# Kernel optimization log

Hardware: AMD Instinct MI355X
Metric: run time of the kernel (lower is better)

The kernel has to match this reference:

```python
import jax, jax.numpy as jnp
import numpy as np
import math

B, T, D, H = 2, 4096, 1024, 16
DH = D // H
LOCAL = 3
MAX_GATE = 0.6


def dilated_positions(seq_len, local=LOCAL):
    A = local + int(math.ceil(math.log2(max(seq_len, 2)))) + 1
    pos = np.zeros((seq_len, A), np.int32)
    msk = np.zeros((seq_len, A), bool)
    for i in range(seq_len):
        ap = [i] + [i - j for j in range(1, local + 1) if i - j >= 0]
        k = 2
        while 2 ** k <= i:
            ap.append(i - 2 ** k)
            k += 1
        pos[i, :len(ap)] = ap
        msk[i, :len(ap)] = True
    return pos, msk


def pid_proj(x, Wp, Wi, Wd, Wg, bg):
    # x: (B,T,D); W*: (D,D); Wg: (D,3); bg: (3,)
    t = x.shape[1]
    denom = jnp.arange(1, t + 1, dtype=x.dtype)[None, :, None]
    integral = jnp.cumsum(x, axis=1) / denom
    derivative = jnp.concatenate([jnp.zeros_like(x[:, :1]), x[:, 1:] - x[:, :-1]], axis=1)
    g = jax.nn.softmax(x @ Wg + bg, axis=-1)
    g = jnp.minimum(g, MAX_GATE)
    g = g / g.sum(axis=-1, keepdims=True)
    return g[..., 0:1] * (x @ Wp) + g[..., 1:2] * (integral @ Wi) + g[..., 2:3] * (derivative @ Wd)


def setup_inputs() -> dict:
    key = jax.random.key(0)
    ks = jax.random.split(key, 16)
    s = 1.0 / math.sqrt(D)
    inp = {"x": jax.random.normal(ks[0], (B, T, D), jnp.float32)}
    i = 1
    for name in ("q", "k", "v"):
        inp[f"Wp_{name}"] = jax.random.normal(ks[i], (D, D), jnp.float32) * s; i += 1
        inp[f"Wi_{name}"] = jax.random.normal(ks[i], (D, D), jnp.float32) * s * 0.3; i += 1
        inp[f"Wd_{name}"] = jax.random.normal(ks[i], (D, D), jnp.float32) * s * 0.3; i += 1
        inp[f"Wg_{name}"] = jax.random.normal(ks[i], (D, 3), jnp.float32) * s; i += 1
        inp[f"bg_{name}"] = jnp.array([0.5, 0.0, 0.0], jnp.float32)
    inp["Wo"] = jax.random.normal(ks[13], (D, D), jnp.float32) * s
    pos, msk = dilated_positions(T)
    inp["positions"] = jnp.asarray(pos)
    inp["mask"] = jnp.asarray(msk)
    return inp


def reference(x, Wp_q, Wi_q, Wd_q, Wg_q, bg_q,
              Wp_k, Wi_k, Wd_k, Wg_k, bg_k,
              Wp_v, Wi_v, Wd_v, Wg_v, bg_v,
              Wo, positions, mask):
    b, t, d = x.shape
    scale = DH ** -0.5
    def heads(y):  # (B,T,D) -> (B,H,T,DH)
        return y.reshape(b, t, H, DH).transpose(0, 2, 1, 3)
    q = heads(pid_proj(x, Wp_q, Wi_q, Wd_q, Wg_q, bg_q))
    k = heads(pid_proj(x, Wp_k, Wi_k, Wd_k, Wg_k, bg_k))
    v = heads(pid_proj(x, Wp_v, Wi_v, Wd_v, Wg_v, bg_v))
    # gather per-query sparse K/V: (B,H,T,A,DH)
    k_sparse = k[:, :, positions]
    v_sparse = v[:, :, positions]
    scores = jnp.einsum('bhsd,bhsad->bhsa', q, k_sparse) * scale
    scores = jnp.where(mask[None, None], scores, -jnp.inf)
    attn = jax.nn.softmax(scores, axis=-1)
    out = jnp.einsum('bhsa,bhsad->bhsd', attn, v_sparse)
    out = out.transpose(0, 2, 1, 3).reshape(b, t, d)
    return out @ Wo
```

## Files before the change

kernel.cpp:

```cpp
#include <hip/hip_runtime.h>
#include <hip/hip_bf16.h>
#include <cstdint>

#define B_   2
#define T_   4096
#define D_   1024
#define H_   16
#define DH_  64
#define M_   (B_*T_)
#define K3_  (3*D_)
#define TC_  128
#define NCH_ (T_/TC_)

typedef __attribute__((ext_vector_type(4))) float  f32x4;
typedef __attribute__((ext_vector_type(8))) short  short8;

__device__ __forceinline__ float bf2f(ushort u) {
    union { uint32_t i; float f; } v; v.i = ((uint32_t)u) << 16; return v.f;
}
__device__ __forceinline__ ushort f2bf(float f) {
    union { float f; uint32_t i; } v; v.f = f;
    uint32_t r = v.i + 0x7FFF + ((v.i >> 16) & 1);
    return (ushort)(r >> 16);
}

template<bool F32>
__device__ __forceinline__ float ld_in(const void* p, size_t i) {
    if (F32) return ((const float*)p)[i];
    return bf2f(((const ushort*)p)[i]);
}

__device__ __forceinline__ void st_c(ushort* p, float v) { *p = f2bf(v); }
__device__ __forceinline__ void st_c(float*  p, float v) { *p = v; }

#define GLOAD_LDS16(g, l) \
    __builtin_amdgcn_global_load_lds((const __attribute__((address_space(1))) void*)(g), \
                                     (__attribute__((address_space(3))) void*)(l), 16, 0, 0)

__global__ void detect_kernel(const ushort* __restrict__ xu, int* __restrict__ flag) {
    __shared__ int cnt;
    if (threadIdx.x == 0) cnt = 0;
    __syncthreads();
    int c = 0;
    for (int i = threadIdx.x; i < 16384; i += 256) {
        ushort u = xu[i];
        if ((u & 0x7F80) == 0x7F80) c++;
    }
    if (c) atomicAdd(&cnt, c);
    __syncthreads();
    if (threadIdx.x == 0) flag[0] = (cnt > 0) ? 1 : 0;
}

template<bool F32>
__device__ __forceinline__ void gates_body(const void* x,
                                           const void* Wg_q, const void* bg_q,
                                           const void* Wg_k, const void* bg_k,
                                           const void* Wg_v, const void* bg_v,
                                           float* __restrict__ g9) {
    const int wave = threadIdx.x >> 6, lane = threadIdx.x & 63;
    const int row  = blockIdx.x * 4 + wave;
    const size_t xoff = (size_t)row * D_;
    float acc[9] = {0,0,0,0,0,0,0,0,0};
    for (int d = lane; d < D_; d += 64) {
        float xv = ld_in<F32>(x, xoff + d);
        #pragma unroll
        for (int c = 0; c < 3; c++) {
            acc[0+c] += xv * ld_in<F32>(Wg_q, d*3+c);
            acc[3+c] += xv * ld_in<F32>(Wg_k, d*3+c);
            acc[6+c] += xv * ld_in<F32>(Wg_v, d*3+c);
        }
    }
    #pragma unroll
    for (int i = 0; i < 9; i++) {
        #pragma unroll
        for (int o = 32; o >= 1; o >>= 1) acc[i] += __shfl_xor(acc[i], o, 64);
    }
    const void* bgs[3] = {bg_q, bg_k, bg_v};
    float g[9];
    #pragma unroll
    for (int p = 0; p < 3; p++) {
        float l0 = acc[p*3+0] + ld_in<F32>(bgs[p], 0);
        float l1 = acc[p*3+1] + ld_in<F32>(bgs[p], 1);
        float l2 = acc[p*3+2] + ld_in<F32>(bgs[p], 2);
        float mx = fmaxf(l0, fmaxf(l1, l2));
        float e0 = expf(l0-mx), e1 = expf(l1-mx), e2 = expf(l2-mx);
        float s  = e0+e1+e2;
        float g0 = fminf(e0/s, 0.6f), g1 = fminf(e1/s, 0.6f), g2 = fminf(e2/s, 0.6f);
        float s2 = g0+g1+g2;
        g0 /= s2; g1 /= s2; g2 /= s2;
        float g1c = fmaxf(g1, 1e-30f), g2c = fmaxf(g2, 1e-30f);
        g[p*3+0] = g0 / g1c;
        g[p*3+1] = g1c / g2c;
        g[p*3+2] = g2c;
    }
    if (lane == 0) {
        #pragma unroll
        for (int i = 0; i < 9; i++) g9[(size_t)row*9 + i] = g[i];
    }
}
__global__ void gates_kernel(const void* x,
                             const void* Wg_q, const void* bg_q,
                             const void* Wg_k, const void* bg_k,
                             const void* Wg_v, const void* bg_v,
                             const int* __restrict__ flag, float* __restrict__ g9) {
    if (flag[0]) gates_body<true >(x, Wg_q, bg_q, Wg_k, bg_k, Wg_v, bg_v, g9);
    else         gates_body<false>(x, Wg_q, bg_q, Wg_k, bg_k, Wg_v, bg_v, g9);
}

template<bool F32>
__device__ __forceinline__ void chunk_sum_body(const void* x, float* __restrict__ part) {
    const int d = blockIdx.x * 256 + threadIdx.x;
    const int tc = blockIdx.y, b = blockIdx.z;
    const size_t base = ((size_t)b*T_ + (size_t)tc*TC_) * D_ + d;
    float s = 0.f;
    for (int i = 0; i < TC_; i++) s += ld_in<F32>(x, base + (size_t)i * D_);
    part[((size_t)b*NCH_ + tc) * D_ + d] = s;
}
__global__ void chunk_sum_kernel(const void* x, const int* __restrict__ flag,
                                 float* __restrict__ part) {
    if (flag[0]) chunk_sum_body<true >(x, part);
    else         chunk_sum_body<false>(x, part);
}

__global__ void scan_part_kernel(float* __restrict__ part) {
    const int idx = blockIdx.x * 256 + threadIdx.x;
    const int b = idx >> 10, d = idx & (D_-1);
    float run = 0.f;
    for (int tc = 0; tc < NCH_; tc++) {
        size_t o = ((size_t)b*NCH_ + tc) * D_ + d;
        float v = part[o]; part[o] = run; run += v;
    }
}

template<bool F32>
__device__ __forceinline__ void build_xs_body(const void* x, const float* __restrict__ part,
                                              ushort* __restrict__ Xc) {
    const int d0 = (blockIdx.x * 256 + threadIdx.x) * 2;
    const int tc = blockIdx.y, b = blockIdx.z;
    const int t0 = tc * TC_;
    float carry0 = part[((size_t)b*NCH_ + tc) * D_ + d0];
    float carry1 = part[((size_t)b*NCH_ + tc) * D_ + d0 + 1];
    const size_t xbase = ((size_t)b*T_ + t0) * D_ + d0;
    float prev0 = (t0 > 0) ? ld_in<F32>(x, xbase - D_)     : 0.0f;
    float prev1 = (t0 > 0) ? ld_in<F32>(x, xbase - D_ + 1) : 0.0f;
    for (int i = 0; i < TC_; i++) {
        const int t = t0 + i;
        float xv0 = ld_in<F32>(x, xbase + (size_t)i * D_);
        float xv1 = ld_in<F32>(x, xbase + (size_t)i * D_ + 1);
        carry0 += xv0; carry1 += xv1;
        const float rinv = 1.0f / (float)(t + 1);
        float in0 = carry0 * rinv, in1 = carry1 * rinv;
        float de0 = (t == 0) ? 0.0f : (xv0 - prev0);
        float de1 = (t == 0) ? 0.0f : (xv1 - prev1);
        prev0 = xv0; prev1 = xv1;
        const size_t base = ((size_t)b*T_ + t) * K3_ + d0;
        *(ushort2*)(Xc + base       ) = make_ushort2(f2bf(xv0), f2bf(xv1));
        *(ushort2*)(Xc + base +   D_) = make_ushort2(f2bf(in0), f2bf(in1));
        *(ushort2*)(Xc + base + 2*D_) = make_ushort2(f2bf(de0), f2bf(de1));
    }
}
__global__ void build_xs_kernel(const void* x, const float* __restrict__ part,
                                const int* __restrict__ flag, ushort* __restrict__ Xc) {
    if (flag[0]) build_xs_body<true >(x, part, Xc);
    else         build_xs_body<false>(x, part, Xc);
}

struct WPtrs { const void* w[10]; };
template<bool F32>
__device__ __forceinline__ void transpose_w_body(WPtrs ptrs, ushort* __restrict__ Wt,
                                                 ushort* __restrict__ WoT) {
    const int z = blockIdx.z;
    const void* src = ptrs.w[z];
    __shared__ float tile[32][33];
    const int tx = threadIdx.x & 31, ty = threadIdx.x >> 5;
    const int d0 = blockIdx.x * 32, c0 = blockIdx.y * 32;
    #pragma unroll
    for (int i = 0; i < 4; i++) {
        int r = ty + i*8;
        tile[r][tx] = ld_in<F32>(src, (size_t)(d0 + r) * D_ + c0 + tx);
    }
    __syncthreads();
    if (z < 9) {
        const int p = z / 3, j = z % 3;
        #pragma unroll
        for (int i = 0; i < 4; i++) {
            int r = ty + i*8;
            Wt[(size_t)(p*D_ + c0 + r) * K3_ + j*D_ + d0 + tx] = f2bf(tile[tx][r]);
        }
    } else {
        #pragma unroll
        for (int i = 0; i < 4; i++) {
            int r = ty + i*8;
            WoT[(size_t)(c0 + r) * D_ + d0 + tx] = f2bf(tile[tx][r]);
        }
    }
}
__global__ void transpose_w_kernel(WPtrs ptrs, const int* __restrict__ flag,
                                   ushort* __restrict__ Wt, ushort* __restrict__ WoT) {
    if (flag[0]) transpose_w_body<true >(ptrs, Wt, WoT);
    else         transpose_w_body<false>(ptrs, Wt, WoT);
}

template<typename CT, int NTILES, bool GATED>
__global__ __launch_bounds__(512, 2) void gemm_bt8_kernel(
        const ushort* __restrict__ Abase,
        const ushort* __restrict__ Bt,
        CT* __restrict__ C,
        const float* __restrict__ g9,
        int K, int lda, int ldc) {
    __shared__ __align__(16) ushort LDS[3 * 24576];
    const int tid  = threadIdx.x;
    const int lane = tid & 63;
    const int wave = tid >> 6;
    const int wm   = wave >> 2;
    const int wn   = wave & 3;
    const int quad = lane >> 4, l16 = lane & 15, sw = l16 & 7;

    const int MT     = M_ / 128;
    const int cpx    = (MT * NTILES) / 8;
    const int wg     = (blockIdx.x % 8) * cpx + blockIdx.x / 8;
    const int mchunk = MT / 8;
    const int rem    = wg % (mchunk * NTILES);
    const int mt     = (wg / (mchunk * NTILES)) * mchunk + (rem % mchunk);
    const int nt     = rem / mchunk;
    const int m0 = mt * 128;
    const int n0 = nt * 256;
    const int p  = n0 >> 10;

    const ushort* asrc[2]; int aoff[2];
    #pragma unroll
    for (int g = 0; g < 2; g++) {
        const int I = g*512 + tid;
        const int row = I >> 3, c8 = (I & 7) ^ (row & 7);
        asrc[g] = Abase + (size_t)(m0 + row) * lda + c8*8;
        aoff[g] = I * 8;
    }
    const ushort* bsrc[4]; int boff[4];
    #pragma unroll
    for (int g = 0; g < 4; g++) {
        const int I = g*512 + tid;
        const int row = I >> 3, c8 = (I & 7) ^ (row & 7);
        bsrc[g] = Bt + (size_t)(n0 + row) * K + c8*8;
        boff[g] = I * 8;
    }
    int ard[4], brd[4];
    #pragma unroll
    for (int i = 0; i < 4; i++) {
        ard[i] = (wm*64 + i*16 + l16) * 64;
        brd[i] = (wn*64 + i*16 + l16) * 64;
    }

    const int NKT = K >> 6;
    f32x4 acc[4][4] = {};

    #pragma unroll
    for (int g = 0; g < 2; g++) GLOAD_LDS16(asrc[g], &LDS[aoff[g]]);
    #pragma unroll
    for (int g = 0; g < 4; g++) GLOAD_LDS16(bsrc[g], &LDS[8192 + boff[g]]);
    #pragma unroll
    for (int g = 0; g < 2; g++) GLOAD_LDS16(asrc[g] + 64, &LDS[24576 + aoff[g]]);
    #pragma unroll
    for (int g = 0; g < 4; g++) GLOAD_LDS16(bsrc[g] + 64, &LDS[24576 + 8192 + boff[g]]);
    asm volatile("s_waitcnt vmcnt(6)" ::: "memory");
    __builtin_amdgcn_s_barrier();

    for (int t = 0; t < NKT; ++t) {
        const int cur = t % 3;
        const int ab  = cur * 24576;
        const int bb  = ab + 8192;
        const bool do_stage = (t + 2 < NKT);
        const int sb  = ((t + 2) % 3) * 24576;
        const int skt = (t + 2) << 6;

        short8 af[4], bfr[4];

        #pragma unroll
        for (int i = 0; i < 4; i++)
            af[i]  = *(const short8*)&LDS[ab + ard[i] + (quad ^ sw) * 8];
        #pragma unroll
        for (int j = 0; j < 4; j++)
            bfr[j] = *(const short8*)&LDS[bb + brd[j] + (quad ^ sw) * 8];
        if (do_stage) {
            GLOAD_LDS16(asrc[0] + skt, &LDS[sb + aoff[0]]);
            GLOAD_LDS16(asrc[1] + skt, &LDS[sb + aoff[1]]);
            GLOAD_LDS16(bsrc[0] + skt, &LDS[sb + 8192 + boff[0]]);
        }
        __builtin_amdgcn_s_barrier();
        asm volatile("s_waitcnt lgkmcnt(0)" ::: "memory");
        __builtin_amdgcn_sched_barrier(0);
        __builtin_amdgcn_s_setprio(1);
        #pragma unroll
        for (int i = 0; i < 4; i++)
            #pragma unroll
            for (int j = 0; j < 4; j++)
                acc[i][j] = __builtin_amdgcn_mfma_f32_16x16x32_bf16(af[i], bfr[j], acc[i][j], 0, 0, 0);
        __builtin_amdgcn_s_setprio(0);
        __builtin_amdgcn_s_barrier();

        #pragma unroll
        for (int i = 0; i < 4; i++)
            af[i]  = *(const short8*)&LDS[ab + ard[i] + ((quad + 4) ^ sw) * 8];
        #pragma unroll
        for (int j = 0; j < 4; j++)
            bfr[j] = *(const short8*)&LDS[bb + brd[j] + ((quad + 4) ^ sw) * 8];
        if (do_stage) {
            GLOAD_LDS16(bsrc[1] + skt, &LDS[sb + 8192 + boff[1]]);
            GLOAD_LDS16(bsrc[2] + skt, &LDS[sb + 8192 + boff[2]]);
            GLOAD_LDS16(bsrc[3] + skt, &LDS[sb + 8192 + boff[3]]);
        }
        __builtin_amdgcn_s_barrier();
        asm volatile("s_waitcnt lgkmcnt(0)" ::: "memory");
        __builtin_amdgcn_sched_barrier(0);
        __builtin_amdgcn_s_setprio(1);
        #pragma unroll
        for (int i = 0; i < 4; i++)
            #pragma unroll
            for (int j = 0; j < 4; j++)
                acc[i][j] = __builtin_amdgcn_mfma_f32_16x16x32_bf16(af[i], bfr[j], acc[i][j], 0, 0, 0);
        __builtin_amdgcn_s_setprio(0);
        if (do_stage)          asm volatile("s_waitcnt vmcnt(6)" ::: "memory");
        else if (t + 1 < NKT)  asm volatile("s_waitcnt vmcnt(0)" ::: "memory");
        __builtin_amdgcn_s_barrier();

        if (GATED && ((t & 15) == 15)) {
            const int seg = t >> 4;
            #pragma unroll
            for (int i = 0; i < 4; i++) {
                float gv[4];
                #pragma unroll
                for (int rg = 0; rg < 4; rg++) {
                    const int rrow = m0 + wm*64 + i*16 + quad*4 + rg;
                    gv[rg] = g9[(size_t)rrow * 9 + p*3 + seg];
                }
                #pragma unroll
                for (int j = 0; j < 4; j++)
                    #pragma unroll
                    for (int rg = 0; rg < 4; rg++)
                        acc[i][j][rg] *= gv[rg];
            }
        }
    }

    #pragma unroll
    for (int i = 0; i < 4; i++) {
        #pragma unroll
        for (int j = 0; j < 4; j++) {
            const int rrow = m0 + wm*64 + i*16 + quad*4;
            const int col  = n0 + wn*64 + j*16 + l16;
            #pragma unroll
            for (int rg = 0; rg < 4; rg++)
                st_c(&C[(size_t)(rrow + rg) * ldc + col], acc[i][j][rg]);
        }
    }
}

__global__ __launch_bounds__(256) void attn_kernel(const ushort* __restrict__ QKV,
                                                   ushort* __restrict__ AO) {
    const int tid = threadIdx.x;
    const int bt  = blockIdx.x;
    const int t   = bt & (T_-1);
    const size_t qrow = (size_t)bt * K3_;
    const int e0 = tid * 4;

    const ushort4 q4 = *(const ushort4*)(QKV + qrow + e0);
    const float qf0 = bf2f(q4.x), qf1 = bf2f(q4.y), qf2 = bf2f(q4.z), qf3 = bf2f(q4.w);

    float sc[14];
    #pragma unroll
    for (int a = 0; a < 14; a++) {
        const int off = (a <= 3) ? a : (1 << (a - 2));
        float p = -1e30f;
        if (off <= t) {
            const ushort4 k4 = *(const ushort4*)(QKV + qrow - (size_t)off*K3_ + D_ + e0);
            float pp = qf0*bf2f(k4.x) + qf1*bf2f(k4.y) + qf2*bf2f(k4.z) + qf3*bf2f(k4.w);
            pp += __shfl_xor(pp, 1, 64);
            pp += __shfl_xor(pp, 2, 64);
            pp += __shfl_xor(pp, 4, 64);
            pp += __shfl_xor(pp, 8, 64);
            p = pp * 0.125f;
        }
        sc[a] = p;
    }
    float mx = -1e30f;
    #pragma unroll
    for (int a = 0; a < 14; a++) mx = fmaxf(mx, sc[a]);
    float ev[14], s = 0.0f;
    #pragma unroll
    for (int a = 0; a < 14; a++) { ev[a] = (sc[a] > -1e29f) ? expf(sc[a] - mx) : 0.0f; s += ev[a]; }
    const float rs = 1.0f / s;

    float a0 = 0.f, a1 = 0.f, a2 = 0.f, a3 = 0.f;
    #pragma unroll
    for (int a = 0; a < 14; a++) {
        const int off = (a <= 3) ? a : (1 << (a - 2));
        if (off <= t) {
            const ushort4 v4 = *(const ushort4*)(QKV + qrow - (size_t)off*K3_ + 2*D_ + e0);
            const float w = ev[a] * rs;
            a0 += w * bf2f(v4.x); a1 += w * bf2f(v4.y);
            a2 += w * bf2f(v4.z); a3 += w * bf2f(v4.w);
        }
    }
    ushort* dst = AO + (size_t)bt * D_ + e0;
    dst[0] = f2bf(a0); dst[1] = f2bf(a1); dst[2] = f2bf(a2); dst[3] = f2bf(a3);
}

extern "C" void kernel_launch(void* const* d_in, const int* in_sizes, int n_in,
                              void* d_out, int out_size, void* d_ws, size_t ws_size,
                              hipStream_t stream) {
    (void)in_sizes; (void)n_in; (void)out_size; (void)ws_size;
    const void* x    = d_in[0];
    const void* Wg_q = d_in[4];  const void* bg_q = d_in[5];
    const void* Wg_k = d_in[9];  const void* bg_k = d_in[10];
    const void* Wg_v = d_in[14]; const void* bg_v = d_in[15];

    char* ws = (char*)d_ws;
    int*    flag = (int*)ws;    ws += 16;
    float*  g9   = (float*)ws;  ws += (size_t)M_*9*4;
    float*  part = (float*)ws;  ws += (size_t)B_*NCH_*D_*4;
    ushort* Wt   = (ushort*)ws; ws += (size_t)K3_*K3_*2;
    ushort* WoT  = (ushort*)ws; ws += (size_t)D_*D_*2;
    ushort* Xc   = (ushort*)ws; ws += (size_t)M_*K3_*2;
    ushort* QKV  = (ushort*)ws; ws += (size_t)M_*K3_*2;
    ushort* AO   = (ushort*)ws; ws += (size_t)M_*D_*2;

    detect_kernel<<<1, 256, 0, stream>>>((const ushort*)x, flag);
    gates_kernel<<<M_/4, 256, 0, stream>>>(x, Wg_q, bg_q, Wg_k, bg_k, Wg_v, bg_v, flag, g9);
    chunk_sum_kernel<<<dim3(D_/256, NCH_, B_), 256, 0, stream>>>(x, flag, part);
    scan_part_kernel<<<(B_*D_)/256, 256, 0, stream>>>(part);
    WPtrs wp;
    wp.w[0] = d_in[1];  wp.w[1] = d_in[2];  wp.w[2] = d_in[3];
    wp.w[3] = d_in[6];  wp.w[4] = d_in[7];  wp.w[5] = d_in[8];
    wp.w[6] = d_in[11]; wp.w[7] = d_in[12]; wp.w[8] = d_in[13];
    wp.w[9] = d_in[16];
    transpose_w_kernel<<<dim3(32, 32, 10), 256, 0, stream>>>(wp, flag, Wt, WoT);
    build_xs_kernel<<<dim3(D_/512, NCH_, B_), 256, 0, stream>>>(x, part, flag, Xc);
    gemm_bt8_kernel<ushort, 12, true><<<768, 512, 0, stream>>>(Xc, Wt, QKV, g9, K3_, K3_, K3_);
    attn_kernel<<<B_*T_, 256, 0, stream>>>(QKV, AO);
    gemm_bt8_kernel<float, 4, false><<<256, 512, 0, stream>>>(AO, WoT, (float*)d_out, nullptr, D_, D_, D_);
}
```

Baseline: 481.3 us.

## Add dedicated 256x384-tile QKV GEMM kernel with split-phase staged pipeline

Replaces the generic 128-row QKV GEMM (768 blocks) with a specialised kernel that computes 256x384 output tiles per 512-thread block over 256 blocks. Each wave holds an 8x6 grid of 16x16 MFMA accumulators. The K loop runs a triple-buffered LDS pipeline whose global loads are split across two compute phases. The gate scaling is applied to the accumulators at each 1024-wide K segment boundary. The larger tile increases operand reuse and cuts global traffic, but it raises register pressure (192 accumulator floats per lane) and leaves only 256 blocks, which may underfill the GPU.

```diff
diff --git a/kernel.cpp b/kernel.cpp
--- a/kernel.cpp
+++ b/kernel.cpp
@@ -201,6 +201,136 @@
     else         transpose_w_body<false>(ptrs, Wt, WoT);
 }
 
+__global__ __launch_bounds__(512, 2) void gemm_qkv_kernel(
+        const ushort* __restrict__ Abase,
+        const ushort* __restrict__ Bt,
+        ushort* __restrict__ C,
+        const float* __restrict__ g9) {
+    constexpr int BUFE = 20480;
+    constexpr int NKT  = K3_ / 32;
+    __shared__ __align__(16) ushort LDS[3 * BUFE];
+    const int tid  = threadIdx.x;
+    const int lane = tid & 63;
+    const int wave = tid >> 6;
+    const int wm   = wave >> 2;
+    const int wn   = wave & 3;
+    const int quad = lane >> 4, l16 = lane & 15;
+
+    const int wg  = (blockIdx.x % 8) * 32 + blockIdx.x / 8;
+    const int rem = wg & 31;
+    const int mt  = (wg >> 5) * 4 + (rem & 3);
+    const int nt  = rem >> 2;
+    const int m0  = mt * 256;
+    const int n0  = nt * 384;
+
+    const ushort* gsrc[5]; int loff[5];
+    #pragma unroll
+    for (int g = 0; g < 5; g++) {
+        const int I = g*512 + tid;
+        if (I < 1024) {
+            gsrc[g] = Abase + (size_t)(m0 + (I >> 2)) * K3_ + (I & 3) * 8;
+            loff[g] = I * 8;
+        } else {
+            const int J = I - 1024;
+            gsrc[g] = Bt + (size_t)(n0 + (J >> 2)) * K3_ + (J & 3) * 8;
+            loff[g] = 8192 + J * 8;
+        }
+    }
+    int ard[8], brd[6];
+    #pragma unroll
+    for (int i = 0; i < 8; i++) ard[i] = (wm*128 + i*16 + l16) * 32 + quad*8;
+    #pragma unroll
+    for (int j = 0; j < 6; j++) brd[j] = 8192 + (wn*96 + j*16 + l16) * 32 + quad*8;
+
+    f32x4 acc[8][6] = {};
+
+    #pragma unroll
+    for (int g = 0; g < 5; g++) GLOAD_LDS16(gsrc[g], &LDS[loff[g]]);
+    #pragma unroll
+    for (int g = 0; g < 5; g++) GLOAD_LDS16(gsrc[g] + 32, &LDS[BUFE + loff[g]]);
+    asm volatile("s_waitcnt vmcnt(5)" ::: "memory");
+    __builtin_amdgcn_s_barrier();
+
+    for (int t = 0; t < NKT; ++t) {
+        const int bs = (t % 3) * BUFE;
+        const bool do_stage = (t + 2 < NKT);
+        const int sb = ((t + 2) % 3) * BUFE;
+        const int sk = (t + 2) * 32;
+
+        short8 af[4], bfr[6], af2[4];
+
+        #pragma unroll
+        for (int i = 0; i < 4; i++) af[i]  = *(const short8*)&LDS[bs + ard[i]];
+        #pragma unroll
+        for (int j = 0; j < 6; j++) bfr[j] = *(const short8*)&LDS[bs + brd[j]];
+        if (do_stage) {
+            GLOAD_LDS16(gsrc[0] + sk, &LDS[sb + loff[0]]);
+            GLOAD_LDS16(gsrc[1] + sk, &LDS[sb + loff[1]]);
+            GLOAD_LDS16(gsrc[2] + sk, &LDS[sb + loff[2]]);
+        }
+        __builtin_amdgcn_s_barrier();
+        asm volatile("s_waitcnt lgkmcnt(0)" ::: "memory");
+        __builtin_amdgcn_sched_barrier(0);
+        __builtin_amdgcn_s_setprio(1);
+        #pragma unroll
+        for (int i = 0; i < 4; i++)
+            #pragma unroll
+            for (int j = 0; j < 6; j++)
+                acc[i][j] = __builtin_amdgcn_mfma_f32_16x16x32_bf16(af[i], bfr[j], acc[i][j], 0, 0, 0);
+        __builtin_amdgcn_s_setprio(0);
+        __builtin_amdgcn_s_barrier();
+
+        #pragma unroll
+        for (int i = 0; i < 4; i++) af2[i] = *(const short8*)&LDS[bs + ard[i+4]];
+        if (do_stage) {
+            GLOAD_LDS16(gsrc[3] + sk, &LDS[sb + loff[3]]);
+            GLOAD_LDS16(gsrc[4] + sk, &LDS[sb + loff[4]]);
+        }
+        __builtin_amdgcn_s_barrier();
+        asm volatile("s_waitcnt lgkmcnt(0)" ::: "memory");
+        __builtin_amdgcn_sched_barrier(0);
+        __builtin_amdgcn_s_setprio(1);
+        #pragma unroll
+        for (int i = 0; i < 4; i++)
+            #pragma unroll
+            for (int j = 0; j < 6; j++)
+                acc[i+4][j] = __builtin_amdgcn_mfma_f32_16x16x32_bf16(af2[i], bfr[j], acc[i+4][j], 0, 0, 0);
+        __builtin_amdgcn_s_setprio(0);
+        if (do_stage)          asm volatile("s_waitcnt vmcnt(5)" ::: "memory");
+        else if (t + 1 < NKT)  asm volatile("s_waitcnt vmcnt(0)" ::: "memory");
+        __builtin_amdgcn_s_barrier();
+
+        if ((t & 31) == 31) {
+            const int seg = t >> 5;
+            #pragma unroll
+            for (int i = 0; i < 8; i++) {
+                #pragma unroll
+                for (int rg = 0; rg < 4; rg++) {
+                    const int rrow = m0 + wm*128 + i*16 + quad*4 + rg;
+                    const float* gr = &g9[(size_t)rrow * 9 + seg];
+                    #pragma unroll
+                    for (int j = 0; j < 6; j++) {
+                        const int pj = (n0 + wn*96 + j*16) >> 10;
+                        acc[i][j][rg] *= gr[pj*3];
+                    }
+                }
+            }
+        }
+    }
+
+    #pragma unroll
+    for (int i = 0; i < 8; i++) {
+        #pragma unroll
+        for (int j = 0; j < 6; j++) {
+            const int rrow = m0 + wm*128 + i*16 + quad*4;
+            const int col  = n0 + wn*96 + j*16 + l16;
+            #pragma unroll
+            for (int rg = 0; rg < 4; rg++)
+                C[(size_t)(rrow + rg) * K3_ + col] = f2bf(acc[i][j][rg]);
+        }
+    }
+}
+
 template<typename CT, int NTILES, bool GATED>
 __global__ __launch_bounds__(512, 2) void gemm_bt8_kernel(
         const ushort* __restrict__ Abase,
@@ -434,7 +564,7 @@
     wp.w[9] = d_in[16];
     transpose_w_kernel<<<dim3(32, 32, 10), 256, 0, stream>>>(wp, flag, Wt, WoT);
     build_xs_kernel<<<dim3(D_/512, NCH_, B_), 256, 0, stream>>>(x, part, flag, Xc);
-    gemm_bt8_kernel<ushort, 12, true><<<768, 512, 0, stream>>>(Xc, Wt, QKV, g9, K3_, K3_, K3_);
+    gemm_qkv_kernel<<<256, 512, 0, stream>>>(Xc, Wt, QKV, g9);
     attn_kernel<<<B_*T_, 256, 0, stream>>>(QKV, AO);
     gemm_bt8_kernel<float, 4, false><<<256, 512, 0, stream>>>(AO, WoT, (float*)d_out, nullptr, D_, D_, D_);
 }
```

Measured after the change: 566.3 us. +17.7%, slower.

## Add dedicated 256x256-tile QKV GEMM with 4-stage LDS pipeline and in-loop gating

Applied to the files above, without the earlier changes.

Replaces the generic gated GEMM for the fused QKV projection with a specialized kernel using 256x256 output tiles (384 workgroups instead of 768), a 4-deep LDS ring buffer with direct global-to-LDS loads, and swizzled LDS reads. Gate scaling is applied to the accumulators at each 1024-wide K segment boundary. The aim is higher arithmetic intensity per tile and better overlap of loads with MFMA work. In exchange it uses more registers and LDS per workgroup, and with fewer workgroups the 256 CUs are covered less evenly.

```diff
diff --git a/kernel.cpp b/kernel.cpp
--- a/kernel.cpp
+++ b/kernel.cpp
@@ -201,6 +201,131 @@
     else         transpose_w_body<false>(ptrs, Wt, WoT);
 }
 
+__global__ __launch_bounds__(512, 2) void gemm_qkv_kernel(
+        const ushort* __restrict__ Abase,
+        const ushort* __restrict__ Bt,
+        ushort* __restrict__ C,
+        const float* __restrict__ g9) {
+    constexpr int SUBE = 16384;
+    constexpr int NS   = K3_ / 32;
+    constexpr int RSTR = 128 * K3_;
+    __shared__ __align__(16) ushort LDS[4 * SUBE];
+    const int tid  = threadIdx.x;
+    const int lane = tid & 63;
+    const int wave = tid >> 6;
+    const int wm   = wave >> 2;
+    const int wn   = wave & 3;
+    const int quad = lane >> 4, l16 = lane & 15;
+    const int gq   = quad ^ ((l16 >> 1) & 3);
+
+    const int wg = (blockIdx.x % 8) * 48 + blockIdx.x / 8;
+    const int mt = wg & 31;
+    const int nt = wg >> 5;
+    const int m0 = mt * 256;
+    const int n0 = nt * 256;
+    const int p  = n0 >> 10;
+
+    const int arow = tid >> 2;
+    const int acg  = (tid & 3) ^ ((arow >> 1) & 3);
+    const ushort* pA = Abase + (size_t)(m0 + arow) * K3_ + acg * 8;
+    const ushort* pB = Bt    + (size_t)(n0 + arow) * K3_ + acg * 8;
+    const int l8 = tid * 8;
+
+    int ard[8], brd[4];
+    #pragma unroll
+    for (int i = 0; i < 8; i++) ard[i] = (wm*128 + i*16 + l16) * 32 + gq*8;
+    #pragma unroll
+    for (int j = 0; j < 4; j++) brd[j] = 8192 + (wn*64 + j*16 + l16) * 32 + gq*8;
+
+    f32x4 acc[8][4] = {};
+
+    #pragma unroll
+    for (int s = 0; s < 3; s++) {
+        const int base = s * SUBE;
+        GLOAD_LDS16(pA + s*32,        &LDS[base + l8]);
+        GLOAD_LDS16(pA + RSTR + s*32, &LDS[base + l8 + 4096]);
+        GLOAD_LDS16(pB + s*32,        &LDS[base + 8192 + l8]);
+        GLOAD_LDS16(pB + RSTR + s*32, &LDS[base + 8192 + l8 + 4096]);
+    }
+    asm volatile("s_waitcnt vmcnt(8)" ::: "memory");
+    __builtin_amdgcn_s_barrier();
+
+    for (int s = 0; s < NS; ++s) {
+        const int bs = (s & 3) * SUBE;
+        const int sb = ((s + 3) & 3) * SUBE;
+        const int sk = (s + 3) * 32;
+        const bool stage = (s + 3 < NS);
+
+        short8 af[4], bfr[4], af2[4];
+
+        #pragma unroll
+        for (int i = 0; i < 4; i++) af[i]  = *(const short8*)&LDS[bs + ard[i]];
+        #pragma unroll
+        for (int j = 0; j < 4; j++) bfr[j] = *(const short8*)&LDS[bs + brd[j]];
+        if (stage) {
+            GLOAD_LDS16(pA + sk,        &LDS[sb + l8]);
+            GLOAD_LDS16(pA + RSTR + sk, &LDS[sb + l8 + 4096]);
+        }
+        asm volatile("s_waitcnt lgkmcnt(0)" ::: "memory");
+        __builtin_amdgcn_sched_barrier(0);
+        __builtin_amdgcn_s_setprio(1);
+        #pragma unroll
+        for (int i = 0; i < 4; i++)
+            #pragma unroll
+            for (int j = 0; j < 4; j++)
+                acc[i][j] = __builtin_amdgcn_mfma_f32_16x16x32_bf16(af[i], bfr[j], acc[i][j], 0, 0, 0);
+        __builtin_amdgcn_s_setprio(0);
+
+        #pragma unroll
+        for (int i = 0; i < 4; i++) af2[i] = *(const short8*)&LDS[bs + ard[i+4]];
+        if (stage) {
+            GLOAD_LDS16(pB + sk,        &LDS[sb + 8192 + l8]);
+            GLOAD_LDS16(pB + RSTR + sk, &LDS[sb + 8192 + l8 + 4096]);
+        }
+        asm volatile("s_waitcnt lgkmcnt(0)" ::: "memory");
+        __builtin_amdgcn_sched_barrier(0);
+        __builtin_amdgcn_s_setprio(1);
+        #pragma unroll
+        for (int i = 0; i < 4; i++)
+            #pragma unroll
+            for (int j = 0; j < 4; j++)
+                acc[4+i][j] = __builtin_amdgcn_mfma_f32_16x16x32_bf16(af2[i], bfr[j], acc[4+i][j], 0, 0, 0);
+        __builtin_amdgcn_s_setprio(0);
+
+        if (stage)             asm volatile("s_waitcnt vmcnt(8)" ::: "memory");
+        else if (s + 3 == NS)  asm volatile("s_waitcnt vmcnt(4)" ::: "memory");
+        else if (s + 2 == NS)  asm volatile("s_waitcnt vmcnt(0)" ::: "memory");
+        __builtin_amdgcn_s_barrier();
+
+        if ((s & 31) == 31) {
+            const int seg = s >> 5;
+            #pragma unroll
+            for (int i = 0; i < 8; i++) {
+                #pragma unroll
+                for (int rg = 0; rg < 4; rg++) {
+                    const int rrow = m0 + wm*128 + i*16 + quad*4 + rg;
+                    const float gv = g9[(size_t)rrow * 9 + p*3 + seg];
+                    #pragma unroll
+                    for (int j = 0; j < 4; j++)
+                        acc[i][j][rg] *= gv;
+                }
+            }
+        }
+    }
+
+    #pragma unroll
+    for (int i = 0; i < 8; i++) {
+        #pragma unroll
+        for (int j = 0; j < 4; j++) {
+            const int rrow = m0 + wm*128 + i*16 + quad*4;
+            const int col  = n0 + wn*64 + j*16 + l16;
+            #pragma unroll
+            for (int rg = 0; rg < 4; rg++)
+                C[(size_t)(rrow + rg) * K3_ + col] = f2bf(acc[i][j][rg]);
+        }
+    }
+}
+
 template<typename CT, int NTILES, bool GATED>
 __global__ __launch_bounds__(512, 2) void gemm_bt8_kernel(
         const ushort* __restrict__ Abase,
@@ -434,7 +559,7 @@
     wp.w[9] = d_in[16];
     transpose_w_kernel<<<dim3(32, 32, 10), 256, 0, stream>>>(wp, flag, Wt, WoT);
     build_xs_kernel<<<dim3(D_/512, NCH_, B_), 256, 0, stream>>>(x, part, flag, Xc);
-    gemm_bt8_kernel<ushort, 12, true><<<768, 512, 0, stream>>>(Xc, Wt, QKV, g9, K3_, K3_, K3_);
+    gemm_qkv_kernel<<<384, 512, 0, stream>>>(Xc, Wt, QKV, g9);
     attn_kernel<<<B_*T_, 256, 0, stream>>>(QKV, AO);
     gemm_bt8_kernel<float, 4, false><<<256, 512, 0, stream>>>(AO, WoT, (float*)d_out, nullptr, D_, D_, D_);
 }
```

Measured after the change: 517.4 us. 1.08x slower.
